# Kernel optimization log

Hardware: AMD Instinct MI355X
Metric: run time of the kernel (lower is better)

Reference implementation:

```python
import jax, jax.numpy as jnp
import numpy as np

PHI = 0.1  # fraction of pruned weights randomized per inference


def setup_inputs() -> dict:
    key = jax.random.key(0)
    k1, k2, k3 = jax.random.split(key, 3)
    d_out, d_in, batch = 8192, 8192, 256
    W = jax.random.normal(k1, (d_out, d_in), jnp.float32) * 0.02
    prune = jax.random.uniform(k2, (d_out, d_in)) < 0.9
    W = jnp.where(prune, 0.0, W)
    mask = (W == 0.0)  # _register_masks: pruned positions
    x = jax.random.normal(k3, (batch, d_in), jnp.float32)
    return {"x": x, "W": W, "mask": mask}


def reference(x, W, mask):
    # --- _apply_random_flip (vectorized) ---
    n_pruned = int(np.asarray(jnp.sum(mask)))          # concrete mask -> static count
    n_flip = max(1, int(PHI * n_pruned))
    keep = ~mask
    n_keep = jnp.sum(keep).astype(W.dtype)
    wk = jnp.where(keep, W, 0.0)
    mean = jnp.sum(wk) / n_keep
    # torch .std() is unbiased (n-1 denominator)
    var = jnp.sum(jnp.where(keep, (W - mean) ** 2, 0.0)) / (n_keep - 1.0)
    std = jnp.sqrt(var)
    key = jax.random.key(42)
    ks, kv = jax.random.split(key)
    # uniform random permutation of pruned indices -> top_k of random scores
    scores = jnp.where(mask.ravel(), jax.random.uniform(ks, (W.size,)), -1.0)
    _, flip_idx = jax.lax.top_k(scores, n_flip)        # [n_flip] flat indices into W
    vals = jax.random.normal(kv, (n_flip,), W.dtype) * std * 0.1
    W_flipped = W.ravel().at[flip_idx].set(vals).reshape(W.shape)
    # --- base_model forward (Linear, no bias) ---
    out = x @ W_flipped.T                               # [batch, d_out]
    # --- _restore_masks: zero flipped weights again (no effect on out) ---
    _ = jnp.where(mask, 0.0, W_flipped)
    return out
```

## Files before the change

### kernel.cpp

```cpp
#include <hip/hip_runtime.h>

typedef unsigned int u32;
typedef unsigned long long u64;
typedef unsigned short u16;
typedef unsigned char u8;

#define NTOT 67108864u
#define NB   8388608u
#define T0   7400000u
#define C0   115625u
#define NBUCK 15447u
#define NBUCKP 16384u
#define CAP  704u
#define KSPLIT 4

struct Scalars {
  double sumW;
  double sumW2;
  u64 npruned;
  u64 nflip;
  float stdf;
  float pad;
};

#define OFF_CNT   0ull
#define OFF_RB    65536ull
#define OFF_SC    131072ull
#define OFF_XBF   131200ull
#define OFF_PAIRS 4325504ull

__host__ __device__ inline void tf2x32(u32 k0, u32 k1, u32 x0, u32 x1, u32& y0, u32& y1) {
  u32 ks2 = k0 ^ k1 ^ 0x1BD11BDAu;
  x0 += k0; x1 += k1;
#define TFR(r) { x0 += x1; x1 = (x1 << (r)) | (x1 >> (32 - (r))); x1 ^= x0; }
  TFR(13) TFR(15) TFR(26) TFR(6)  x0 += k1;  x1 += ks2 + 1u;
  TFR(17) TFR(29) TFR(16) TFR(24) x0 += ks2; x1 += k0 + 2u;
  TFR(13) TFR(15) TFR(26) TFR(6)  x0 += k0;  x1 += k1 + 3u;
  TFR(17) TFR(29) TFR(16) TFR(24) x0 += k1;  x1 += ks2 + 4u;
  TFR(13) TFR(15) TFR(26) TFR(6)  x0 += ks2; x1 += k0 + 5u;
#undef TFR
  y0 = x0; y1 = x1;
}

__device__ inline u32 jax_bits32(u32 k0, u32 k1, u32 i) {
  u32 y0, y1; tf2x32(k0, k1, 0u, i, y0, y1);
  return y0 ^ y1;
}

__device__ inline u16 f2bf(float f) {
  union { float f; u32 u; } c; c.f = f;
  u32 r = ((c.u >> 16) & 1u) + 0x7FFFu;
  return (u16)((c.u + r) >> 16);
}

__device__ inline float erfinv32(float x) {
  float w = -log1pf(-x * x);
  float p;
  if (w < 5.0f) {
    w -= 2.5f;
    p = 2.81022636e-08f;
    p = fmaf(p, w, 3.43273939e-07f);
    p = fmaf(p, w, -3.5233877e-06f);
    p = fmaf(p, w, -4.39150654e-06f);
    p = fmaf(p, w, 0.00021858087f);
    p = fmaf(p, w, -0.00125372503f);
    p = fmaf(p, w, -0.00417768164f);
    p = fmaf(p, w, 0.246640727f);
    p = fmaf(p, w, 1.50140941f);
  } else {
    w = sqrtf(w) - 3.0f;
    p = -0.000200214257f;
    p = fmaf(p, w, 0.000100950558f);
    p = fmaf(p, w, 0.00134934322f);
    p = fmaf(p, w, -0.00367342844f);
    p = fmaf(p, w, 0.00573950773f);
    p = fmaf(p, w, -0.0076224613f);
    p = fmaf(p, w, 0.00943887047f);
    p = fmaf(p, w, 1.00167406f);
    p = fmaf(p, w, 2.83297682f);
  }
  return p * x;
}

__global__ __launch_bounds__(256) void k_pass1(const float* __restrict__ W, Scalars* sc,
                                               u32* cnt, u32* pairs, u32 uk0, u32 uk1) {
  u32 gid = blockIdx.x * blockDim.x + threadIdx.x;
  u32 stride = gridDim.x * blockDim.x;
  u32 lane = threadIdx.x & 63;
  double s = 0.0, s2 = 0.0; u32 c = 0;
  for (u32 l = gid; l < NTOT; l += stride) {
    float w = W[l];
    u32 bits = jax_bits32(uk0, uk1, l);
    s  += (double)w;
    s2 += (double)w * w;
    bool p = (w == 0.0f);
    c += p ? 1u : 0u;
    u32 ub = bits >> 9;
    if (p && ub >= T0) {
      u32 cb = (ub >> 6) - C0;
      u32 pos = atomicAdd(&cnt[cb], 1u);
      if (pos < CAP) pairs[(u64)cb * CAP + pos] = ((ub & 63u) << 26) | l;
    }
  }
  for (int o = 32; o > 0; o >>= 1) {
    s += __shfl_down(s, o); s2 += __shfl_down(s2, o); c += __shfl_down(c, o);
  }
  if (lane == 0) {
    atomicAdd(&sc->sumW, s);
    atomicAdd(&sc->sumW2, s2);
    atomicAdd(&sc->npruned, (u64)c);
  }
}

__global__ void k_pass2(Scalars* sc) {
  double nk = (double)NTOT - (double)sc->npruned;
  double mean = sc->sumW / nk;
  double var = (sc->sumW2 - 2.0 * mean * sc->sumW + nk * mean * mean) / (nk - 1.0);
  sc->stdf = (float)sqrt(var);
  u64 nfi = (u64)(0.1 * (double)sc->npruned);
  if (nfi < 1) nfi = 1;
  sc->nflip = nfi;
}

__global__ __launch_bounds__(256) void k_bscan(const u32* __restrict__ cnt, u32* rb) {
  __shared__ u32 part[256];
  __shared__ u32 off[256];
  u32 t = threadIdx.x;
  u32 base = t * 64;
  u32 s = 0;
  for (int j = 0; j < 64; j++) { u32 v = cnt[base + j]; s += (v > CAP ? CAP : v); }
  part[t] = s;
  __syncthreads();
  if (t == 0) { u32 a = 0; for (int i = 255; i >= 0; i--) { off[i] = a; a += part[i]; } }
  __syncthreads();
  u32 a = off[t];
  for (int j = 63; j >= 0; j--) {
    u32 v = cnt[base + j]; v = (v > CAP ? CAP : v);
    rb[base + j] = a; a += v;
  }
}

__global__ __launch_bounds__(256) void k_rank(float* __restrict__ W,
                                              const u32* __restrict__ cnt,
                                              const u32* __restrict__ rb,
                                              const u32* __restrict__ pairs,
                                              const Scalars* __restrict__ sc,
                                              u32 vk0, u32 vk1) {
  u32 b = blockIdx.x;
  u32 n = cnt[b]; if (n > CAP) n = CAP;
  if (n == 0) return;
  u64 nflip = sc->nflip;
  u32 base = rb[b];
  if ((u64)base >= nflip) return;
  __shared__ u32 sIdx[CAP];
  __shared__ u8  sFine[CAP];
  __shared__ u32 pIdx[CAP];
  __shared__ u32 hist[64];
  __shared__ u32 gbase[64];
  __shared__ u32 cur[64];
  if (threadIdx.x < 64) hist[threadIdx.x] = 0;
  __syncthreads();
  const u32* slice = pairs + (u64)b * CAP;
  for (u32 i = threadIdx.x; i < n; i += 256) {
    u32 e = slice[i];
    u32 fi = e >> 26;
    sIdx[i] = e & 0x03FFFFFFu;
    sFine[i] = (u8)fi;
    atomicAdd(&hist[fi], 1u);
  }
  __syncthreads();
  if (threadIdx.x == 0) {
    u32 a = 0;
    for (int f = 63; f >= 0; f--) { gbase[f] = a; cur[f] = a; a += hist[f]; }
  }
  __syncthreads();
  for (u32 i = threadIdx.x; i < n; i += 256) {
    u32 p = atomicAdd(&cur[sFine[i]], 1u);
    pIdx[p] = sIdx[i];
  }
  __syncthreads();
  float stdf = sc->stdf;
  for (u32 i = threadIdx.x; i < n; i += 256) {
    u32 f = sFine[i];
    u32 g0 = gbase[f], g1 = g0 + hist[f];
    u32 v = sIdx[i];
    u32 ord = 0;
    for (u32 q = g0; q < g1; q++) ord += (pIdx[q] < v) ? 1u : 0u;
    u64 rank = (u64)base + gbase[f] + ord;
    if (rank >= nflip) continue;
    u32 bits = jax_bits32(vk0, vk1, (u32)rank);
    union { u32 u; float fl; } cv; cv.u = 0x3F800000u | (bits >> 9);
    float fu = cv.fl - 1.0f;
    const float lo = -0.99999994f;
    float u2 = fmaxf(lo, fu * 2.0f + lo);
    float nrm = 1.41421354f * erfinv32(u2);
    W[v] = (nrm * stdf) * 0.1f;
  }
}

__global__ __launch_bounds__(256) void k_xconv(const float* __restrict__ x, u16* __restrict__ xbf) {
  u32 i = blockIdx.x * blockDim.x + threadIdx.x;
  float4 v = ((const float4*)x)[i];
  ushort4 o; o.x = f2bf(v.x); o.y = f2bf(v.y); o.z = f2bf(v.z); o.w = f2bf(v.w);
  ((ushort4*)xbf)[i] = o;
}

typedef __bf16 bf16x8 __attribute__((ext_vector_type(8)));
typedef float f32x4 __attribute__((ext_vector_type(4)));

__global__ __launch_bounds__(256, 2) void k_gemm(const u16* __restrict__ xbf,
                                                 const float* __restrict__ W,
                                                 float* __restrict__ out) {
  __shared__ u16 xs[256 * 72];
  __shared__ u16 wsm[64 * 72];
  u32 tid = threadIdx.x;
  u32 lane = tid & 63, wv = tid >> 6;
  u32 nt0 = blockIdx.x * 64;
  u32 kbase = blockIdx.y * (8192 / KSPLIT);
  f32x4 acc[4][4];
#pragma unroll
  for (int i = 0; i < 4; i++)
#pragma unroll
    for (int j = 0; j < 4; j++) acc[i][j] = (f32x4){0.f, 0.f, 0.f, 0.f};

  for (u32 kb = kbase; kb < kbase + 2048u; kb += 64u) {
#pragma unroll
    for (int r8 = 0; r8 < 8; r8++) {
      u32 row = r8 * 32 + (tid >> 3);
      u32 kseg = (tid & 7) * 8;
      uint4 v = *(const uint4*)(xbf + (u64)row * 8192 + kb + kseg);
      *(uint4*)&xs[row * 72 + kseg] = v;
    }
#pragma unroll
    for (int r = 0; r < 4; r++) {
      u32 f4 = r * 256 + tid;
      u32 row = f4 >> 4;
      u32 kc = (f4 & 15) * 4;
      float4 v = *(const float4*)(W + (u64)(nt0 + row) * 8192 + kb + kc);
      ushort4 o; o.x = f2bf(v.x); o.y = f2bf(v.y); o.z = f2bf(v.z); o.w = f2bf(v.w);
      *(ushort4*)&wsm[row * 72 + kc] = o;
    }
    __syncthreads();
#pragma unroll
    for (int ks = 0; ks < 2; ks++) {
      bf16x8 a[4], b[4];
      u32 koff = ks * 32 + (lane >> 4) * 8;
      u32 rsel = lane & 15;
#pragma unroll
      for (int mt = 0; mt < 4; mt++) a[mt] = *(bf16x8*)&xs[(wv * 64 + mt * 16 + rsel) * 72 + koff];
#pragma unroll
      for (int nt = 0; nt < 4; nt++) b[nt] = *(bf16x8*)&wsm[(nt * 16 + rsel) * 72 + koff];
#pragma unroll
      for (int mt = 0; mt < 4; mt++)
#pragma unroll
        for (int nt = 0; nt < 4; nt++)
          acc[mt][nt] = __builtin_amdgcn_mfma_f32_16x16x32_bf16(a[mt], b[nt], acc[mt][nt], 0, 0, 0);
    }
    __syncthreads();
  }
  u32 quad = lane >> 4, col = lane & 15;
#pragma unroll
  for (int mt = 0; mt < 4; mt++)
#pragma unroll
    for (int nt = 0; nt < 4; nt++) {
      u32 n = nt0 + nt * 16 + col;
#pragma unroll
      for (int rg = 0; rg < 4; rg++) {
        u32 m = wv * 64 + mt * 16 + quad * 4 + rg;
        atomicAdd(&out[(u64)m * 8192 + n], acc[mt][nt][rg]);
      }
    }
}

extern "C" void kernel_launch(void* const* d_in, const int* in_sizes, int n_in,
                              void* d_out, int out_size, void* d_ws, size_t ws_size,
                              hipStream_t stream) {
  const float* x; float* W;
  if (in_sizes[0] == 2097152) { x = (const float*)d_in[0]; W = (float*)d_in[1]; }
  else                        { x = (const float*)d_in[1]; W = (float*)d_in[0]; }
  float* out = (float*)d_out;
  char* ws = (char*)d_ws;

  u32* cnt    = (u32*)(ws + OFF_CNT);
  u32* rb     = (u32*)(ws + OFF_RB);
  Scalars* sc = (Scalars*)(ws + OFF_SC);
  u16* xbf    = (u16*)(ws + OFF_XBF);
  u32* pairs  = (u32*)(ws + OFF_PAIRS);

  u32 a0, a1, b0, b1;
  tf2x32(0u, 42u, 0u, 0u, a0, a1);
  tf2x32(0u, 42u, 0u, 1u, b0, b1);

  hipMemsetAsync(cnt, 0, (size_t)NBUCKP * 4, stream);
  hipMemsetAsync(sc, 0, sizeof(Scalars), stream);
  hipMemsetAsync(out, 0, (size_t)out_size * 4, stream);

  k_xconv<<<2048, 256, 0, stream>>>(x, xbf);
  k_pass1<<<2048, 256, 0, stream>>>(W, sc, cnt, pairs, a0, a1);
  k_pass2<<<1, 1, 0, stream>>>(sc);
  k_bscan<<<1, 256, 0, stream>>>(cnt, rb);
  k_rank<<<NBUCK, 256, 0, stream>>>(W, cnt, rb, pairs, sc, b0, b1);
  dim3 g(128, KSPLIT);
  k_gemm<<<g, 256, 0, stream>>>(xbf, W, out);
}
```

Before: 1.166 ms.

## Replace global bucket atomics with per-block segments and routed superbuckets

Candidate selection for the top-k flip no longer does per-element global atomics into 15k fine buckets. Each block now appends candidates to its own segment using a wave ballot and builds a shared-memory histogram. A new routing kernel scatters candidates into 966 coarse superbuckets, and rank blocks recompute the random bits to sort within each one. This trades contended global atomics for an extra routing pass, recomputing the hash, and large shared-memory buffers, with capacity limits per segment and superbucket.

```diff
diff --git a/kernel.cpp b/kernel.cpp
--- a/kernel.cpp
+++ b/kernel.cpp
@@ -3,15 +3,14 @@
 typedef unsigned int u32;
 typedef unsigned long long u64;
 typedef unsigned short u16;
-typedef unsigned char u8;
-
-#define NTOT 67108864u
-#define NB   8388608u
-#define T0   7400000u
-#define C0   115625u
-#define NBUCK 15447u
-#define NBUCKP 16384u
-#define CAP  704u
+
+#define NTOT   67108864u
+#define T0P    7399424u
+#define PBASE  7226u
+#define NSUP   966u
+#define SEGN   2048u
+#define SEGCAP 4096u
+#define SUPCAP 8192u
 #define KSPLIT 4
 
 struct Scalars {
@@ -23,11 +22,15 @@
   float pad;
 };
 
-#define OFF_CNT   0ull
-#define OFF_RB    65536ull
-#define OFF_SC    131072ull
-#define OFF_XBF   131200ull
-#define OFF_PAIRS 4325504ull
+#define OFF_GHIST  0ull
+#define OFF_ALLOC  4096ull
+#define OFF_SBASE  8192ull
+#define OFF_SCUR   12288ull
+#define OFF_SC     16384ull
+#define OFF_SEGCNT 16512ull
+#define OFF_XBF    24704ull
+#define OFF_SEGS   4219008ull
+#define OFF_ROUTED 37773440ull
 
 __host__ __device__ inline void tf2x32(u32 k0, u32 k1, u32 x0, u32 x1, u32& y0, u32& y1) {
   u32 ks2 = k0 ^ k1 ^ 0x1BD11BDAu;
@@ -82,111 +85,220 @@
   return p * x;
 }
 
+__device__ inline void blk_excl_scan_1024(const u32* cnt, u32* excl, u32* wtmp) {
+  __syncthreads();
+  u32 t = threadIdx.x;
+  u32 a0 = cnt[t*4], a1 = cnt[t*4+1], a2 = cnt[t*4+2], a3 = cnt[t*4+3];
+  u32 s = a0 + a1 + a2 + a3;
+  u32 lane = t & 63, wv = t >> 6;
+  u32 inc = s;
+  for (int o = 1; o < 64; o <<= 1) { u32 v = (u32)__shfl_up((int)inc, o); if (lane >= (u32)o) inc += v; }
+  if (lane == 63) wtmp[wv] = inc;
+  __syncthreads();
+  u32 woff = 0;
+  for (u32 w = 0; w < wv; w++) woff += wtmp[w];
+  u32 base = woff + inc - s;
+  excl[t*4]   = base;
+  excl[t*4+1] = base + a0;
+  excl[t*4+2] = base + a0 + a1;
+  excl[t*4+3] = base + a0 + a1 + a2;
+  __syncthreads();
+}
+
+__device__ inline void blk_suffix_scan_1024(const u32* cnt, u32* suf, u32* wtmp) {
+  __syncthreads();
+  u32 t = threadIdx.x;
+  u32 a0 = cnt[1023 - t*4], a1 = cnt[1022 - t*4], a2 = cnt[1021 - t*4], a3 = cnt[1020 - t*4];
+  u32 s = a0 + a1 + a2 + a3;
+  u32 lane = t & 63, wv = t >> 6;
+  u32 inc = s;
+  for (int o = 1; o < 64; o <<= 1) { u32 v = (u32)__shfl_up((int)inc, o); if (lane >= (u32)o) inc += v; }
+  if (lane == 63) wtmp[wv] = inc;
+  __syncthreads();
+  u32 woff = 0;
+  for (u32 w = 0; w < wv; w++) woff += wtmp[w];
+  u32 base = woff + inc - s;
+  suf[1023 - t*4] = base;
+  suf[1022 - t*4] = base + a0;
+  suf[1021 - t*4] = base + a1 + a0;
+  suf[1020 - t*4] = base + a2 + a1 + a0;
+  __syncthreads();
+}
+
 __global__ __launch_bounds__(256) void k_pass1(const float* __restrict__ W, Scalars* sc,
-                                               u32* cnt, u32* pairs, u32 uk0, u32 uk1) {
-  u32 gid = blockIdx.x * blockDim.x + threadIdx.x;
-  u32 stride = gridDim.x * blockDim.x;
+                                               u32* ghist, u32* segcnt, u32* segs,
+                                               u32 uk0, u32 uk1) {
+  __shared__ u32 lhist[1024];
+  __shared__ u32 lcnt, lwr;
+  for (u32 j = threadIdx.x; j < 1024; j += 256) lhist[j] = 0;
+  if (threadIdx.x == 0) { lcnt = 0; lwr = 0; }
+  __syncthreads();
+  u32 gid = blockIdx.x * 256 + threadIdx.x;
+  u32 stride4 = SEGN * 256 * 4;
   u32 lane = threadIdx.x & 63;
-  double s = 0.0, s2 = 0.0; u32 c = 0;
-  for (u32 l = gid; l < NTOT; l += stride) {
-    float w = W[l];
-    u32 bits = jax_bits32(uk0, uk1, l);
-    s  += (double)w;
-    s2 += (double)w * w;
-    bool p = (w == 0.0f);
-    c += p ? 1u : 0u;
-    u32 ub = bits >> 9;
-    if (p && ub >= T0) {
-      u32 cb = (ub >> 6) - C0;
-      u32 pos = atomicAdd(&cnt[cb], 1u);
-      if (pos < CAP) pairs[(u64)cb * CAP + pos] = ((ub & 63u) << 26) | l;
+  u64 lt = (lane == 0) ? 0ull : (~0ull >> (64 - lane));
+  u32* seg = segs + (u64)blockIdx.x * SEGCAP;
+  double s = 0.0, s2 = 0.0; u32 cnt = 0;
+  for (u32 b4 = gid * 4; b4 < NTOT; b4 += stride4) {
+    float4 wv4 = *(const float4*)(W + b4);
+    float we[4] = {wv4.x, wv4.y, wv4.z, wv4.w};
+#pragma unroll
+    for (int e = 0; e < 4; e++) {
+      u32 l = b4 + e;
+      float w = we[e];
+      s  += (double)w;
+      s2 += (double)w * w;
+      bool pr = (w == 0.0f);
+      cnt += pr ? 1u : 0u;
+      u32 sb = jax_bits32(uk0, uk1, l) >> 9;
+      bool q = pr && (sb >= T0P);
+      u64 m = __ballot(q);
+      u32 tot = (u32)__popcll(m);
+      if (tot) {
+        u32 base = 0;
+        if (lane == 0) base = atomicAdd(&lcnt, tot);
+        base = (u32)__shfl((int)base, 0);
+        if (base + tot <= SEGCAP) {
+          if (lane == 0) atomicMax(&lwr, base + tot);
+          if (q) {
+            seg[base + (u32)__popcll(m & lt)] = l;
+            atomicAdd(&lhist[(sb >> 10) - PBASE], 1u);
+          }
+        }
+      }
     }
   }
   for (int o = 32; o > 0; o >>= 1) {
-    s += __shfl_down(s, o); s2 += __shfl_down(s2, o); c += __shfl_down(c, o);
+    s += __shfl_down(s, o); s2 += __shfl_down(s2, o); cnt += __shfl_down(cnt, o);
   }
   if (lane == 0) {
     atomicAdd(&sc->sumW, s);
     atomicAdd(&sc->sumW2, s2);
-    atomicAdd(&sc->npruned, (u64)c);
-  }
-}
-
-__global__ void k_pass2(Scalars* sc) {
-  double nk = (double)NTOT - (double)sc->npruned;
-  double mean = sc->sumW / nk;
-  double var = (sc->sumW2 - 2.0 * mean * sc->sumW + nk * mean * mean) / (nk - 1.0);
-  sc->stdf = (float)sqrt(var);
-  u64 nfi = (u64)(0.1 * (double)sc->npruned);
-  if (nfi < 1) nfi = 1;
-  sc->nflip = nfi;
-}
-
-__global__ __launch_bounds__(256) void k_bscan(const u32* __restrict__ cnt, u32* rb) {
-  __shared__ u32 part[256];
-  __shared__ u32 off[256];
+    atomicAdd(&sc->npruned, (u64)cnt);
+  }
+  __syncthreads();
+  for (u32 j = threadIdx.x; j < 1024; j += 256)
+    if (j < NSUP && lhist[j]) atomicAdd(&ghist[j], lhist[j]);
+  if (threadIdx.x == 0) segcnt[blockIdx.x] = lwr;
+}
+
+__global__ __launch_bounds__(256) void k_scan(const u32* __restrict__ ghist, Scalars* sc,
+                                              u32* alloc, u32* superbase, u32* supercur) {
+  __shared__ u32 h[1024], ex[1024], sb[1024], wtmp[4];
   u32 t = threadIdx.x;
-  u32 base = t * 64;
-  u32 s = 0;
-  for (int j = 0; j < 64; j++) { u32 v = cnt[base + j]; s += (v > CAP ? CAP : v); }
-  part[t] = s;
-  __syncthreads();
-  if (t == 0) { u32 a = 0; for (int i = 255; i >= 0; i--) { off[i] = a; a += part[i]; } }
-  __syncthreads();
-  u32 a = off[t];
-  for (int j = 63; j >= 0; j--) {
-    u32 v = cnt[base + j]; v = (v > CAP ? CAP : v);
-    rb[base + j] = a; a += v;
+  for (u32 j = t; j < 1024; j += 256) h[j] = ghist[j];
+  blk_excl_scan_1024(h, ex, wtmp);
+  blk_suffix_scan_1024(h, sb, wtmp);
+  for (u32 j = t; j < 1024; j += 256) {
+    alloc[j] = ex[j]; superbase[j] = sb[j]; supercur[j] = ex[j];
+  }
+  if (t == 0) {
+    double nk = (double)NTOT - (double)sc->npruned;
+    double mean = sc->sumW / nk;
+    double var = (sc->sumW2 - 2.0 * mean * sc->sumW + nk * mean * mean) / (nk - 1.0);
+    sc->stdf = (float)sqrt(var);
+    u64 nfi = (u64)(0.1 * (double)sc->npruned);
+    if (nfi < 1) nfi = 1;
+    sc->nflip = nfi;
+  }
+}
+
+__global__ __launch_bounds__(256) void k_route(const u32* __restrict__ segs,
+                                               const u32* __restrict__ segcnt,
+                                               u32* supercur, u32* routed,
+                                               u32 uk0, u32 uk1) {
+  __shared__ u32 lbuf[16384];
+  __shared__ u16 lp[16384];
+  __shared__ u16 inv[16384];
+  __shared__ u32 lhist[1024], lbase[1024], gdest[1024], lcur[1024];
+  __shared__ u32 wtmp[4];
+  u32 t = threadIdx.x;
+  for (u32 j = t; j < 1024; j += 256) lhist[j] = 0;
+  u32 c0 = segcnt[blockIdx.x*4+0], c1 = segcnt[blockIdx.x*4+1];
+  u32 c2 = segcnt[blockIdx.x*4+2], c3 = segcnt[blockIdx.x*4+3];
+  u32 off[4] = {0, c0, c0+c1, c0+c1+c2};
+  u32 cs[4] = {c0, c1, c2, c3};
+  u32 total = c0+c1+c2+c3;
+  __syncthreads();
+#pragma unroll
+  for (int sg = 0; sg < 4; sg++) {
+    const u32* sp = segs + ((u64)blockIdx.x*4 + sg) * SEGCAP;
+    for (u32 i = t; i < cs[sg]; i += 256) {
+      u32 idx = sp[i];
+      u32 sb2 = jax_bits32(uk0, uk1, idx) >> 9;
+      u32 p = (sb2 >> 10) - PBASE;
+      u32 j = off[sg] + i;
+      lbuf[j] = idx;
+      lp[j] = (u16)p;
+      atomicAdd(&lhist[p], 1u);
+    }
+  }
+  blk_excl_scan_1024(lhist, lbase, wtmp);
+  for (u32 p = t; p < 1024; p += 256) {
+    u32 c = lhist[p];
+    if (c) gdest[p] = atomicAdd(&supercur[p], c);
+    lcur[p] = lbase[p];
+  }
+  __syncthreads();
+  for (u32 j = t; j < total; j += 256) {
+    u32 slot = atomicAdd(&lcur[lp[j]], 1u);
+    inv[slot] = (u16)j;
+  }
+  __syncthreads();
+  for (u32 j = t; j < total; j += 256) {
+    u32 i = inv[j];
+    u32 p = lp[i];
+    routed[gdest[p] + (j - lbase[p])] = lbuf[i];
   }
 }
 
 __global__ __launch_bounds__(256) void k_rank(float* __restrict__ W,
-                                              const u32* __restrict__ cnt,
-                                              const u32* __restrict__ rb,
-                                              const u32* __restrict__ pairs,
+                                              const u32* __restrict__ ghist,
+                                              const u32* __restrict__ alloc,
+                                              const u32* __restrict__ superbase,
+                                              const u32* __restrict__ routed,
                                               const Scalars* __restrict__ sc,
-                                              u32 vk0, u32 vk1) {
-  u32 b = blockIdx.x;
-  u32 n = cnt[b]; if (n > CAP) n = CAP;
-  if (n == 0) return;
+                                              u32 uk0, u32 uk1, u32 vk0, u32 vk1) {
+  u32 p = blockIdx.x;
+  u32 n = ghist[p]; if (n == 0) return;
+  if (n > SUPCAP) n = SUPCAP;
   u64 nflip = sc->nflip;
-  u32 base = rb[b];
-  if ((u64)base >= nflip) return;
-  __shared__ u32 sIdx[CAP];
-  __shared__ u8  sFine[CAP];
-  __shared__ u32 pIdx[CAP];
-  __shared__ u32 hist[64];
-  __shared__ u32 gbase[64];
-  __shared__ u32 cur[64];
-  if (threadIdx.x < 64) hist[threadIdx.x] = 0;
-  __syncthreads();
-  const u32* slice = pairs + (u64)b * CAP;
-  for (u32 i = threadIdx.x; i < n; i += 256) {
-    u32 e = slice[i];
-    u32 fi = e >> 26;
-    sIdx[i] = e & 0x03FFFFFFu;
-    sFine[i] = (u8)fi;
-    atomicAdd(&hist[fi], 1u);
-  }
-  __syncthreads();
-  if (threadIdx.x == 0) {
-    u32 a = 0;
-    for (int f = 63; f >= 0; f--) { gbase[f] = a; cur[f] = a; a += hist[f]; }
-  }
-  __syncthreads();
-  for (u32 i = threadIdx.x; i < n; i += 256) {
-    u32 p = atomicAdd(&cur[sFine[i]], 1u);
-    pIdx[p] = sIdx[i];
+  u32 rbase = superbase[p];
+  if ((u64)rbase >= nflip) return;
+  __shared__ u32 sIdx[SUPCAP];
+  __shared__ u16 sFine[SUPCAP];
+  __shared__ u32 pIdx[SUPCAP];
+  __shared__ u32 hist[1024], gbase[1024], cur[1024];
+  __shared__ u32 wtmp[4];
+  u32 t = threadIdx.x;
+  for (u32 j = t; j < 1024; j += 256) hist[j] = 0;
+  __syncthreads();
+  const u32* src = routed + alloc[p];
+  u32 fbias = (p + PBASE) << 10;
+  for (u32 i = t; i < n; i += 256) {
+    u32 idx = src[i];
+    u32 sb2 = jax_bits32(uk0, uk1, idx) >> 9;
+    u32 f = sb2 - fbias;
+    sIdx[i] = idx;
+    sFine[i] = (u16)f;
+    atomicAdd(&hist[f], 1u);
+  }
+  blk_suffix_scan_1024(hist, gbase, wtmp);
+  for (u32 j = t; j < 1024; j += 256) cur[j] = gbase[j];
+  __syncthreads();
+  for (u32 i = t; i < n; i += 256) {
+    u32 pos = atomicAdd(&cur[sFine[i]], 1u);
+    pIdx[pos] = sIdx[i];
   }
   __syncthreads();
   float stdf = sc->stdf;
-  for (u32 i = threadIdx.x; i < n; i += 256) {
+  for (u32 i = t; i < n; i += 256) {
     u32 f = sFine[i];
     u32 g0 = gbase[f], g1 = g0 + hist[f];
     u32 v = sIdx[i];
     u32 ord = 0;
     for (u32 q = g0; q < g1; q++) ord += (pIdx[q] < v) ? 1u : 0u;
-    u64 rank = (u64)base + gbase[f] + ord;
+    u64 rank = (u64)rbase + gbase[f] + ord;
     if (rank >= nflip) continue;
     u32 bits = jax_bits32(vk0, vk1, (u32)rank);
     union { u32 u; float fl; } cv; cv.u = 0x3F800000u | (bits >> 9);
@@ -281,25 +393,29 @@
   float* out = (float*)d_out;
   char* ws = (char*)d_ws;
 
-  u32* cnt    = (u32*)(ws + OFF_CNT);
-  u32* rb     = (u32*)(ws + OFF_RB);
-  Scalars* sc = (Scalars*)(ws + OFF_SC);
-  u16* xbf    = (u16*)(ws + OFF_XBF);
-  u32* pairs  = (u32*)(ws + OFF_PAIRS);
+  u32* ghist     = (u32*)(ws + OFF_GHIST);
+  u32* alloc     = (u32*)(ws + OFF_ALLOC);
+  u32* superbase = (u32*)(ws + OFF_SBASE);
+  u32* supercur  = (u32*)(ws + OFF_SCUR);
+  Scalars* sc    = (Scalars*)(ws + OFF_SC);
+  u32* segcnt    = (u32*)(ws + OFF_SEGCNT);
+  u16* xbf       = (u16*)(ws + OFF_XBF);
+  u32* segs      = (u32*)(ws + OFF_SEGS);
+  u32* routed    = (u32*)(ws + OFF_ROUTED);
 
   u32 a0, a1, b0, b1;
   tf2x32(0u, 42u, 0u, 0u, a0, a1);
   tf2x32(0u, 42u, 0u, 1u, b0, b1);
 
-  hipMemsetAsync(cnt, 0, (size_t)NBUCKP * 4, stream);
+  hipMemsetAsync(ghist, 0, 4096, stream);
   hipMemsetAsync(sc, 0, sizeof(Scalars), stream);
   hipMemsetAsync(out, 0, (size_t)out_size * 4, stream);
 
   k_xconv<<<2048, 256, 0, stream>>>(x, xbf);
-  k_pass1<<<2048, 256, 0, stream>>>(W, sc, cnt, pairs, a0, a1);
-  k_pass2<<<1, 1, 0, stream>>>(sc);
-  k_bscan<<<1, 256, 0, stream>>>(cnt, rb);
-  k_rank<<<NBUCK, 256, 0, stream>>>(W, cnt, rb, pairs, sc, b0, b1);
+  k_pass1<<<SEGN, 256, 0, stream>>>(W, sc, ghist, segcnt, segs, a0, a1);
+  k_scan<<<1, 256, 0, stream>>>(ghist, sc, alloc, superbase, supercur);
+  k_route<<<SEGN / 4, 256, 0, stream>>>(segs, segcnt, supercur, routed, a0, a1);
+  k_rank<<<NSUP, 256, 0, stream>>>(W, ghist, alloc, superbase, routed, sc, a0, a1, b0, b1);
   dim3 g(128, KSPLIT);
   k_gemm<<<g, 256, 0, stream>>>(xbf, W, out);
 }
```

Result: no change. 1.153 ms (-1.1%).
